# Kernel tuning notes

Hardware: AMD Instinct MI355X
Metric: run time of the kernel (lower is better)

## Reference

```python
import jax, jax.numpy as jnp
import numpy as np

N = 50000      # drug nodes
E = 600000     # edges (avg degree 12)
D = 128        # emb_dim
HOPS = 2       # n_hops
NEFF = 1000    # n_effects
Q = 200000     # number of (node, effect) query pairs


def setup_inputs() -> dict:
    key = jax.random.key(0)
    ks = jax.random.split(key, 9)
    graph_x = jax.random.normal(ks[0], (N, D), dtype=jnp.float32)
    edge_index = jax.random.randint(ks[1], (2, E), 0, N)
    chemical_similarity = jax.random.uniform(ks[2], (E,), dtype=jnp.float32)
    x_nodes = jax.random.randint(ks[3], (Q,), 0, N)
    effect_ids = jax.random.randint(ks[4], (Q,), 0, NEFF)
    # per-hop SAGEConv params: self transform, neighbor transform, bias
    W_self = jax.random.normal(ks[5], (HOPS, D, D), dtype=jnp.float32) / np.sqrt(D)
    W_neigh = jax.random.normal(ks[6], (HOPS, D, D), dtype=jnp.float32) / np.sqrt(D)
    bias = jnp.zeros((HOPS, D), dtype=jnp.float32)
    # xavier-uniform effect embedding table
    lim = np.sqrt(6.0 / (NEFF + D))
    effect_emb = jax.random.uniform(ks[7], (NEFF, D), dtype=jnp.float32, minval=-lim, maxval=lim)
    return {
        "graph_x": graph_x,
        "edge_index": edge_index,
        "x_nodes": x_nodes,
        "effect_ids": effect_ids,
        "chemical_similarity": chemical_similarity,
        "W_self": W_self,
        "W_neigh": W_neigh,
        "bias": bias,
        "effect_emb": effect_emb,
    }


def reference(graph_x, edge_index, x_nodes, effect_ids, chemical_similarity,
              W_self, W_neigh, bias, effect_emb):
    src, dst = edge_index[0], edge_index[1]
    w = chemical_similarity  # [E]
    x = graph_x              # [N, D]
    for h in range(HOPS):
        # weighted-mean neighbor aggregation (SAGEConv with edge weights)
        msg = x[src] * w[:, None]                                  # [E, D]
        agg = jax.ops.segment_sum(msg, dst, num_segments=N)        # [N, D]
        denom = jax.ops.segment_sum(w, dst, num_segments=N)        # [N]
        agg = agg / jnp.maximum(denom, 1e-12)[:, None]
        x = jax.nn.relu(x @ W_self[h] + agg @ W_neigh[h] + bias[h])
    # final gather + effect embedding add
    return x[x_nodes] + effect_emb[effect_ids]                     # [Q, D]
```

## Files before the change

### kernel.cpp

```cpp
#include <hip/hip_runtime.h>
#include <hip/hip_bf16.h>

#define D 128
#define CAP 64
#define BM 64
#define CSTR 32

using bf16x8 = __attribute__((ext_vector_type(8))) short;
using f32x4  = __attribute__((ext_vector_type(4))) float;

static __device__ __forceinline__ unsigned short f2bf(float f) {
    unsigned u = __float_as_uint(f);
    u += 0x7FFF + ((u >> 16) & 1);
    return (unsigned short)(u >> 16);
}
static __device__ __forceinline__ float bf2f(unsigned short s) {
    return __uint_as_float(((unsigned)s) << 16);
}

__global__ __launch_bounds__(256) void prep_fused(
    const float* __restrict__ xin, ushort* __restrict__ xb,
    const float* __restrict__ Ws, const float* __restrict__ Wn,
    ushort* __restrict__ Wt, int* __restrict__ cnt,
    long n8, int wtot, int nzero4, int nConv, int nWt)
{
    const int b = blockIdx.x;
    if (b < nConv) {
        long i = (long)b * 256 + threadIdx.x;
        if (i >= n8) return;
        const float4* p = (const float4*)xin + i * 2;
        float4 a = p[0], v = p[1];
        uint4 o;
        o.x = (unsigned)f2bf(a.x) | ((unsigned)f2bf(a.y) << 16);
        o.y = (unsigned)f2bf(a.z) | ((unsigned)f2bf(a.w) << 16);
        o.z = (unsigned)f2bf(v.x) | ((unsigned)f2bf(v.y) << 16);
        o.w = (unsigned)f2bf(v.z) | ((unsigned)f2bf(v.w) << 16);
        ((uint4*)xb)[i] = o;
    } else if (b < nConv + nWt) {
        int idx = (b - nConv) * 256 + threadIdx.x;
        if (idx >= wtot) return;
        int h   = idx >> 15;
        int rem = idx & 32767;
        int n   = rem >> 8;
        int k   = rem & 255;
        float v = (k < D) ? Ws[(size_t)h * D * D + (size_t)k * D + n]
                          : Wn[(size_t)h * D * D + (size_t)(k - D) * D + n];
        Wt[idx] = f2bf(v);
    } else {
        int idx = (b - nConv - nWt) * 256 + threadIdx.x;
        if (idx >= nzero4) return;
        int4 z = {0, 0, 0, 0};
        ((int4*)cnt)[idx] = z;
    }
}

__global__ __launch_bounds__(256) void fill_edges(
    const int* __restrict__ ei, const float* __restrict__ w,
    int* __restrict__ cnt, int2* __restrict__ pad, int E)
{
    int e = blockIdx.x * 256 + threadIdx.x;
    if (e >= E) return;
    int s = ei[e];
    int d = ei[E + e];
    float wv = w[e];
    int pos = atomicAdd(&cnt[(size_t)d * CSTR], 1);
    if (pos < CAP) {
        pad[(size_t)d * CAP + pos] = make_int2(s, __float_as_int(wv));
    }
}

__global__ __launch_bounds__(256) void aggregate(
    const ushort* __restrict__ x, const int* __restrict__ cnt,
    const int2* __restrict__ pad, ushort* __restrict__ agg, int N)
{
    const int wave = threadIdx.x >> 6;
    const int lane = threadIdx.x & 63;
    const int n = blockIdx.x * 4 + wave;
    if (n >= N) return;
    const int c  = lane & 31;
    const int jj = lane >> 5;

    int deg = cnt[(size_t)n * CSTR];
    if (deg > CAP) deg = CAP;
    const size_t base = (size_t)n * CAP;

    float ax = 0.f, ay = 0.f, az = 0.f, aw = 0.f, wsum = 0.f;

    for (int t = 0; t < deg; t += 8) {
        const int j = t + jj * 4;
        int4 p01 = *(const int4*)(pad + base + j);
        int4 p23 = *(const int4*)(pad + base + j + 2);
        const int s0 = (j + 0 < deg) ? p01.x : 0;
        const int s1 = (j + 1 < deg) ? p01.z : 0;
        const int s2 = (j + 2 < deg) ? p23.x : 0;
        const int s3 = (j + 3 < deg) ? p23.z : 0;
        const float w0 = (j + 0 < deg) ? __int_as_float(p01.y) : 0.f;
        const float w1 = (j + 1 < deg) ? __int_as_float(p01.w) : 0.f;
        const float w2 = (j + 2 < deg) ? __int_as_float(p23.y) : 0.f;
        const float w3 = (j + 3 < deg) ? __int_as_float(p23.w) : 0.f;
        ushort4 v0 = *((const ushort4*)(x + (size_t)s0 * D) + c);
        ushort4 v1 = *((const ushort4*)(x + (size_t)s1 * D) + c);
        ushort4 v2 = *((const ushort4*)(x + (size_t)s2 * D) + c);
        ushort4 v3 = *((const ushort4*)(x + (size_t)s3 * D) + c);
        ax += w0 * bf2f(v0.x) + w1 * bf2f(v1.x) + w2 * bf2f(v2.x) + w3 * bf2f(v3.x);
        ay += w0 * bf2f(v0.y) + w1 * bf2f(v1.y) + w2 * bf2f(v2.y) + w3 * bf2f(v3.y);
        az += w0 * bf2f(v0.z) + w1 * bf2f(v1.z) + w2 * bf2f(v2.z) + w3 * bf2f(v3.z);
        aw += w0 * bf2f(v0.w) + w1 * bf2f(v1.w) + w2 * bf2f(v2.w) + w3 * bf2f(v3.w);
        wsum += w0 + w1 + w2 + w3;
    }

    ax += __shfl_xor(ax, 32, 64);
    ay += __shfl_xor(ay, 32, 64);
    az += __shfl_xor(az, 32, 64);
    aw += __shfl_xor(aw, 32, 64);
    wsum += __shfl_xor(wsum, 32, 64);

    if (jj == 0) {
        const float inv = 1.f / fmaxf(wsum, 1e-12f);
        ushort4 o;
        o.x = f2bf(ax * inv); o.y = f2bf(ay * inv);
        o.z = f2bf(az * inv); o.w = f2bf(aw * inv);
        *((ushort4*)(agg + (size_t)n * D) + c) = o;
    }
}

__global__ __launch_bounds__(256) void gemm_mfma(
    const ushort* __restrict__ xin, const ushort* __restrict__ agg,
    const ushort* __restrict__ Wt, const float* __restrict__ bias,
    ushort* __restrict__ xout, int nrows)
{
    __shared__ ushort As[BM][72];
    __shared__ ushort Bs[D][72];
    const int tid  = threadIdx.x;
    const int w    = tid >> 6;
    const int lane = tid & 63;
    const int r16  = lane & 15;
    const int kq   = lane >> 4;
    const int row0 = blockIdx.x * BM;

    f32x4 acc[8];
    #pragma unroll
    for (int nf = 0; nf < 8; ++nf) acc[nf] = {0.f, 0.f, 0.f, 0.f};

    for (int kc = 0; kc < 4; ++kc) {
        {
            const ushort* src = (kc < 2) ? xin : agg;
            const int kb = (kc & 1) * 64;
            const int r = tid >> 2, q = tid & 3;
            const int grow = row0 + r;
            if (grow < nrows) {
                const uint4* gp = (const uint4*)(src + (size_t)grow * D + kb + q * 16);
                uint4 v0 = gp[0], v1 = gp[1];
                *(uint4*)&As[r][q * 16]     = v0;
                *(uint4*)&As[r][q * 16 + 8] = v1;
            } else {
                uint4 z = {0u, 0u, 0u, 0u};
                *(uint4*)&As[r][q * 16]     = z;
                *(uint4*)&As[r][q * 16 + 8] = z;
            }
        }
        {
            const int n = tid >> 1, h2 = tid & 1;
            const uint4* gp = (const uint4*)(Wt + (size_t)n * 256 + kc * 64 + h2 * 32);
            uint4 v0 = gp[0], v1 = gp[1], v2 = gp[2], v3 = gp[3];
            *(uint4*)&Bs[n][h2 * 32]      = v0;
            *(uint4*)&Bs[n][h2 * 32 + 8]  = v1;
            *(uint4*)&Bs[n][h2 * 32 + 16] = v2;
            *(uint4*)&Bs[n][h2 * 32 + 24] = v3;
        }
        __syncthreads();
        #pragma unroll
        for (int kk = 0; kk < 64; kk += 32) {
            bf16x8 a = *(const bf16x8*)&As[w * 16 + r16][kk + kq * 8];
            #pragma unroll
            for (int nf = 0; nf < 8; ++nf) {
                bf16x8 b = *(const bf16x8*)&Bs[nf * 16 + r16][kk + kq * 8];
                acc[nf] = __builtin_amdgcn_mfma_f32_16x16x32_bf16(a, b, acc[nf], 0, 0, 0);
            }
        }
        __syncthreads();
    }
    #pragma unroll
    for (int nf = 0; nf < 8; ++nf) {
        const int col = nf * 16 + r16;
        const float bv = bias[col];
        #pragma unroll
        for (int i = 0; i < 4; ++i) {
            const int grow = row0 + w * 16 + kq * 4 + i;
            if (grow < nrows) {
                float v = fmaxf(acc[nf][i] + bv, 0.f);
                xout[(size_t)grow * D + col] = f2bf(v);
            }
        }
    }
}

__global__ __launch_bounds__(256) void out_kernel(
    const ushort* __restrict__ x, const float* __restrict__ emb,
    const int* __restrict__ xn, const int* __restrict__ eid,
    float* __restrict__ out, int Q)
{
    long g = (long)blockIdx.x * 256 + threadIdx.x;
    long tot = (long)Q * 32;
    if (g >= tot) return;
    int q = (int)(g >> 5);
    int c = (int)(g & 31);
    int nq = xn[q], ef = eid[q];
    ushort4 xv = *((const ushort4*)(x + (size_t)nq * D) + c);
    float4  ev = *((const float4*)(emb + (size_t)ef * D) + c);
    float4 o = {bf2f(xv.x) + ev.x, bf2f(xv.y) + ev.y,
                bf2f(xv.z) + ev.z, bf2f(xv.w) + ev.w};
    ((float4*)out)[g] = o;
}

extern "C" void kernel_launch(void* const* d_in, const int* in_sizes, int n_in,
                              void* d_out, int out_size, void* d_ws, size_t ws_size,
                              hipStream_t stream)
{
    const float* graph_x   = (const float*)d_in[0];
    const int*   edge_idx  = (const int*)d_in[1];
    const int*   x_nodes   = (const int*)d_in[2];
    const int*   effect_id = (const int*)d_in[3];
    const float* chem      = (const float*)d_in[4];
    const float* W_self    = (const float*)d_in[5];
    const float* W_neigh   = (const float*)d_in[6];
    const float* bias      = (const float*)d_in[7];
    const float* eff_emb   = (const float*)d_in[8];

    const int N    = in_sizes[0] / D;
    const int E    = in_sizes[4];
    const int Q    = in_sizes[2];
    const int HOPS = in_sizes[7] / D;

    char* wsp = (char*)d_ws;
    int*    cnt  = (int*)wsp;     wsp += (size_t)N * CSTR * 4;
    int2*   pad  = (int2*)wsp;    wsp += (size_t)N * CAP * 8;
    ushort* xb   = (ushort*)wsp;  wsp += (size_t)N * D * 2;
    ushort* aggb = (ushort*)wsp;  wsp += (size_t)N * D * 2;
    ushort* x1b  = (ushort*)wsp;  wsp += (size_t)N * D * 2;
    ushort* Wt   = (ushort*)wsp;  wsp += (size_t)HOPS * D * 256 * 2;

    const long n8     = (long)N * D / 8;
    const int  wtot   = HOPS * D * 256;
    const int  nzero4 = N * CSTR / 4;
    const int  nConv  = (int)((n8 + 255) / 256);
    const int  nWt    = (wtot + 255) / 256;
    const int  nZero  = (nzero4 + 255) / 256;
    prep_fused<<<nConv + nWt + nZero, 256, 0, stream>>>(
        graph_x, xb, W_self, W_neigh, Wt, cnt, n8, wtot, nzero4, nConv, nWt);

    fill_edges<<<(E + 255) / 256, 256, 0, stream>>>(
        edge_idx, chem, cnt, pad, E);

    const int aggGrid  = (N + 3) / 4;
    const int gemmGrid = (N + BM - 1) / BM;

    for (int h = 0; h < HOPS; ++h) {
        const ushort* xin = (h == 0) ? xb : x1b;
        aggregate<<<aggGrid, 256, 0, stream>>>(xin, cnt, pad, aggb, N);
        gemm_mfma<<<gemmGrid, 256, 0, stream>>>(
            xin, aggb, Wt + (size_t)h * D * 256, bias + (size_t)h * D, x1b, N);
    }

    long tot = (long)Q * 32;
    out_kernel<<<(int)((tot + 255) / 256), 256, 0, stream>>>(
        x1b, eff_emb, x_nodes, effect_id, (float*)d_out, Q);
}
```

Measured before the change: 148.3 us.

## Fuse neighbor aggregation into the SAGE GEMM kernel via shared-memory tile

Merges the separate aggregate and GEMM kernels into one. Each block first gathers the weighted-mean neighbor features for its 64 rows into a shared-memory tile, then feeds that tile directly to the MFMA loop for the neighbor half of K. This removes the global write and read of the aggregated buffer and one launch per hop. A third activation buffer is added because the fused kernel reads other rows of its input while writing output. The trade-off is parallelism: the gather now runs with only 781 blocks, 16 rows per wave done serially, instead of 12500 blocks, and the extra shared memory may lower occupancy.

```diff
diff --git a/kernel.cpp b/kernel.cpp
--- a/kernel.cpp
+++ b/kernel.cpp
@@ -69,68 +69,14 @@
     }
 }
 
-__global__ __launch_bounds__(256) void aggregate(
-    const ushort* __restrict__ x, const int* __restrict__ cnt,
-    const int2* __restrict__ pad, ushort* __restrict__ agg, int N)
-{
-    const int wave = threadIdx.x >> 6;
-    const int lane = threadIdx.x & 63;
-    const int n = blockIdx.x * 4 + wave;
-    if (n >= N) return;
-    const int c  = lane & 31;
-    const int jj = lane >> 5;
-
-    int deg = cnt[(size_t)n * CSTR];
-    if (deg > CAP) deg = CAP;
-    const size_t base = (size_t)n * CAP;
-
-    float ax = 0.f, ay = 0.f, az = 0.f, aw = 0.f, wsum = 0.f;
-
-    for (int t = 0; t < deg; t += 8) {
-        const int j = t + jj * 4;
-        int4 p01 = *(const int4*)(pad + base + j);
-        int4 p23 = *(const int4*)(pad + base + j + 2);
-        const int s0 = (j + 0 < deg) ? p01.x : 0;
-        const int s1 = (j + 1 < deg) ? p01.z : 0;
-        const int s2 = (j + 2 < deg) ? p23.x : 0;
-        const int s3 = (j + 3 < deg) ? p23.z : 0;
-        const float w0 = (j + 0 < deg) ? __int_as_float(p01.y) : 0.f;
-        const float w1 = (j + 1 < deg) ? __int_as_float(p01.w) : 0.f;
-        const float w2 = (j + 2 < deg) ? __int_as_float(p23.y) : 0.f;
-        const float w3 = (j + 3 < deg) ? __int_as_float(p23.w) : 0.f;
-        ushort4 v0 = *((const ushort4*)(x + (size_t)s0 * D) + c);
-        ushort4 v1 = *((const ushort4*)(x + (size_t)s1 * D) + c);
-        ushort4 v2 = *((const ushort4*)(x + (size_t)s2 * D) + c);
-        ushort4 v3 = *((const ushort4*)(x + (size_t)s3 * D) + c);
-        ax += w0 * bf2f(v0.x) + w1 * bf2f(v1.x) + w2 * bf2f(v2.x) + w3 * bf2f(v3.x);
-        ay += w0 * bf2f(v0.y) + w1 * bf2f(v1.y) + w2 * bf2f(v2.y) + w3 * bf2f(v3.y);
-        az += w0 * bf2f(v0.z) + w1 * bf2f(v1.z) + w2 * bf2f(v2.z) + w3 * bf2f(v3.z);
-        aw += w0 * bf2f(v0.w) + w1 * bf2f(v1.w) + w2 * bf2f(v2.w) + w3 * bf2f(v3.w);
-        wsum += w0 + w1 + w2 + w3;
-    }
-
-    ax += __shfl_xor(ax, 32, 64);
-    ay += __shfl_xor(ay, 32, 64);
-    az += __shfl_xor(az, 32, 64);
-    aw += __shfl_xor(aw, 32, 64);
-    wsum += __shfl_xor(wsum, 32, 64);
-
-    if (jj == 0) {
-        const float inv = 1.f / fmaxf(wsum, 1e-12f);
-        ushort4 o;
-        o.x = f2bf(ax * inv); o.y = f2bf(ay * inv);
-        o.z = f2bf(az * inv); o.w = f2bf(aw * inv);
-        *((ushort4*)(agg + (size_t)n * D) + c) = o;
-    }
-}
-
-__global__ __launch_bounds__(256) void gemm_mfma(
-    const ushort* __restrict__ xin, const ushort* __restrict__ agg,
-    const ushort* __restrict__ Wt, const float* __restrict__ bias,
-    ushort* __restrict__ xout, int nrows)
+__global__ __launch_bounds__(256) void gemm_agg(
+    const ushort* __restrict__ xin, const int* __restrict__ cnt,
+    const int2* __restrict__ pad, const ushort* __restrict__ Wt,
+    const float* __restrict__ bias, ushort* __restrict__ xout, int nrows)
 {
     __shared__ ushort As[BM][72];
     __shared__ ushort Bs[D][72];
+    __shared__ ushort Agg[BM][136];
     const int tid  = threadIdx.x;
     const int w    = tid >> 6;
     const int lane = tid & 63;
@@ -138,18 +84,72 @@
     const int kq   = lane >> 4;
     const int row0 = blockIdx.x * BM;
 
+    {
+        const int c  = lane & 31;
+        const int jj = lane >> 5;
+        for (int i = 0; i < 16; ++i) {
+            const int r = w * 16 + i;
+            const int n = row0 + r;
+            if (n >= nrows) {
+                if (jj == 0) {
+                    ushort4 z = {0, 0, 0, 0};
+                    *((ushort4*)&Agg[r][0] + c) = z;
+                }
+                continue;
+            }
+            int deg = cnt[(size_t)n * CSTR];
+            if (deg > CAP) deg = CAP;
+            const size_t base = (size_t)n * CAP;
+
+            float ax = 0.f, ay = 0.f, az = 0.f, aw = 0.f, wsum = 0.f;
+            for (int t = 0; t < deg; t += 8) {
+                const int j = t + jj * 4;
+                int4 p01 = *(const int4*)(pad + base + j);
+                int4 p23 = *(const int4*)(pad + base + j + 2);
+                const int s0 = (j + 0 < deg) ? p01.x : 0;
+                const int s1 = (j + 1 < deg) ? p01.z : 0;
+                const int s2 = (j + 2 < deg) ? p23.x : 0;
+                const int s3 = (j + 3 < deg) ? p23.z : 0;
+                const float w0 = (j + 0 < deg) ? __int_as_float(p01.y) : 0.f;
+                const float w1 = (j + 1 < deg) ? __int_as_float(p01.w) : 0.f;
+                const float w2 = (j + 2 < deg) ? __int_as_float(p23.y) : 0.f;
+                const float w3 = (j + 3 < deg) ? __int_as_float(p23.w) : 0.f;
+                ushort4 v0 = *((const ushort4*)(xin + (size_t)s0 * D) + c);
+                ushort4 v1 = *((const ushort4*)(xin + (size_t)s1 * D) + c);
+                ushort4 v2 = *((const ushort4*)(xin + (size_t)s2 * D) + c);
+                ushort4 v3 = *((const ushort4*)(xin + (size_t)s3 * D) + c);
+                ax += w0 * bf2f(v0.x) + w1 * bf2f(v1.x) + w2 * bf2f(v2.x) + w3 * bf2f(v3.x);
+                ay += w0 * bf2f(v0.y) + w1 * bf2f(v1.y) + w2 * bf2f(v2.y) + w3 * bf2f(v3.y);
+                az += w0 * bf2f(v0.z) + w1 * bf2f(v1.z) + w2 * bf2f(v2.z) + w3 * bf2f(v3.z);
+                aw += w0 * bf2f(v0.w) + w1 * bf2f(v1.w) + w2 * bf2f(v2.w) + w3 * bf2f(v3.w);
+                wsum += w0 + w1 + w2 + w3;
+            }
+            ax += __shfl_xor(ax, 32, 64);
+            ay += __shfl_xor(ay, 32, 64);
+            az += __shfl_xor(az, 32, 64);
+            aw += __shfl_xor(aw, 32, 64);
+            wsum += __shfl_xor(wsum, 32, 64);
+            if (jj == 0) {
+                const float inv = 1.f / fmaxf(wsum, 1e-12f);
+                ushort4 o;
+                o.x = f2bf(ax * inv); o.y = f2bf(ay * inv);
+                o.z = f2bf(az * inv); o.w = f2bf(aw * inv);
+                *((ushort4*)&Agg[r][0] + c) = o;
+            }
+        }
+    }
+
     f32x4 acc[8];
     #pragma unroll
     for (int nf = 0; nf < 8; ++nf) acc[nf] = {0.f, 0.f, 0.f, 0.f};
 
     for (int kc = 0; kc < 4; ++kc) {
-        {
-            const ushort* src = (kc < 2) ? xin : agg;
-            const int kb = (kc & 1) * 64;
+        if (kc < 2) {
+            const int kb = kc * 64;
             const int r = tid >> 2, q = tid & 3;
             const int grow = row0 + r;
             if (grow < nrows) {
-                const uint4* gp = (const uint4*)(src + (size_t)grow * D + kb + q * 16);
+                const uint4* gp = (const uint4*)(xin + (size_t)grow * D + kb + q * 16);
                 uint4 v0 = gp[0], v1 = gp[1];
                 *(uint4*)&As[r][q * 16]     = v0;
                 *(uint4*)&As[r][q * 16 + 8] = v1;
@@ -171,7 +171,11 @@
         __syncthreads();
         #pragma unroll
         for (int kk = 0; kk < 64; kk += 32) {
-            bf16x8 a = *(const bf16x8*)&As[w * 16 + r16][kk + kq * 8];
+            bf16x8 a;
+            if (kc < 2)
+                a = *(const bf16x8*)&As[w * 16 + r16][kk + kq * 8];
+            else
+                a = *(const bf16x8*)&Agg[w * 16 + r16][(kc - 2) * 64 + kk + kq * 8];
             #pragma unroll
             for (int nf = 0; nf < 8; ++nf) {
                 bf16x8 b = *(const bf16x8*)&Bs[nf * 16 + r16][kk + kq * 8];
@@ -236,8 +240,8 @@
     int*    cnt  = (int*)wsp;     wsp += (size_t)N * CSTR * 4;
     int2*   pad  = (int2*)wsp;    wsp += (size_t)N * CAP * 8;
     ushort* xb   = (ushort*)wsp;  wsp += (size_t)N * D * 2;
-    ushort* aggb = (ushort*)wsp;  wsp += (size_t)N * D * 2;
     ushort* x1b  = (ushort*)wsp;  wsp += (size_t)N * D * 2;
+    ushort* x2b  = (ushort*)wsp;  wsp += (size_t)N * D * 2;
     ushort* Wt   = (ushort*)wsp;  wsp += (size_t)HOPS * D * 256 * 2;
 
     const long n8     = (long)N * D / 8;
@@ -252,17 +256,17 @@
     fill_edges<<<(E + 255) / 256, 256, 0, stream>>>(
         edge_idx, chem, cnt, pad, E);
 
-    const int aggGrid  = (N + 3) / 4;
+    ushort* bufs[3] = {xb, x1b, x2b};
     const int gemmGrid = (N + BM - 1) / BM;
-
     for (int h = 0; h < HOPS; ++h) {
-        const ushort* xin = (h == 0) ? xb : x1b;
-        aggregate<<<aggGrid, 256, 0, stream>>>(xin, cnt, pad, aggb, N);
-        gemm_mfma<<<gemmGrid, 256, 0, stream>>>(
-            xin, aggb, Wt + (size_t)h * D * 256, bias + (size_t)h * D, x1b, N);
-    }
+        const ushort* xin = bufs[h];
+        ushort* xout      = bufs[h + 1 == 3 ? 1 : h + 1];
+        gemm_agg<<<gemmGrid, 256, 0, stream>>>(
+            xin, cnt, pad, Wt + (size_t)h * D * 256, bias + (size_t)h * D, xout, N);
+    }
+    const ushort* xfin = bufs[HOPS == 1 ? 1 : (HOPS % 2 == 0 ? 2 : 1)];
 
     long tot = (long)Q * 32;
     out_kernel<<<(int)((tot + 255) / 256), 256, 0, stream>>>(
-        x1b, eff_emb, x_nodes, effect_id, (float*)d_out, Q);
-}
+        xfin, eff_emb, x_nodes, effect_id, (float*)d_out, Q);
+}
```

Result: slower. 229.9 us (+55.1%).
